# Kernel tuning notes

Measured on AMD Instinct MI355X. Metric: run time of the kernel, lower is better.

Reference implementation:

```python
import jax, jax.numpy as jnp
import numpy as np

B, Hg, Wg, DIM, HEADS, WS, SHIFT = 16, 64, 64, 512, 16, 8, 4
HIDDEN = 4 * DIM
PRIOR_BETA = 1.0
EPS = 1e-5


def _layernorm(x, g, b):
    m = jnp.mean(x, axis=-1, keepdims=True)
    v = jnp.mean(jnp.square(x - m), axis=-1, keepdims=True)
    return (x - m) / jnp.sqrt(v + EPS) * g + b


def _rel_pos_index(ws):
    coords = np.stack(np.meshgrid(np.arange(ws), np.arange(ws), indexing='ij')).reshape(2, -1)
    rel = (coords[:, :, None] - coords[:, None, :]).transpose(1, 2, 0)
    rel[..., 0] += ws - 1
    rel[..., 1] += ws - 1
    rel[..., 0] *= 2 * ws - 1
    return rel.sum(-1)  # (N, N) int


def _shift_mask(H, W, ws, shift):
    img = np.zeros((H, W))
    cnt = 0
    for hs in (slice(0, -ws), slice(-ws, -shift), slice(-shift, None)):
        for wsl in (slice(0, -ws), slice(-ws, -shift), slice(-shift, None)):
            img[hs, wsl] = cnt
            cnt += 1
    N = ws * ws
    mw = img.reshape(H // ws, ws, W // ws, ws).transpose(0, 2, 1, 3).reshape(-1, N)
    am = mw[:, None, :] - mw[:, :, None]
    return np.where(am != 0, -100.0, 0.0).astype(np.float32)  # (nW, N, N)


def setup_inputs() -> dict:
    key = jax.random.key(0)
    ks = jax.random.split(key, 8)
    s = 0.02
    return {
        'x': jax.random.normal(ks[0], (B, Hg * Wg, DIM), jnp.float32),
        'M_map': jax.random.uniform(ks[1], (B, Hg, Wg, 1), jnp.float32),
        'norm1_g': jnp.ones((DIM,), jnp.float32),
        'norm1_b': jnp.zeros((DIM,), jnp.float32),
        'qkv_w': jax.random.normal(ks[2], (3 * DIM, DIM), jnp.float32) * s,
        'qkv_b': jnp.zeros((3 * DIM,), jnp.float32),
        'proj_w': jax.random.normal(ks[3], (DIM, DIM), jnp.float32) * s,
        'proj_b': jnp.zeros((DIM,), jnp.float32),
        'rpb_table': jax.random.normal(ks[4], ((2 * WS - 1) ** 2, HEADS), jnp.float32) * s,
        'norm2_g': jnp.ones((DIM,), jnp.float32),
        'norm2_b': jnp.zeros((DIM,), jnp.float32),
        'fc1_w': jax.random.normal(ks[5], (HIDDEN, DIM), jnp.float32) * s,
        'fc1_b': jnp.zeros((HIDDEN,), jnp.float32),
        'fc2_w': jax.random.normal(ks[6], (DIM, HIDDEN), jnp.float32) * s,
        'fc2_b': jnp.zeros((DIM,), jnp.float32),
        'H': Hg,
        'W': Wg,
    }


def reference(x, M_map, norm1_g, norm1_b, qkv_w, qkv_b, proj_w, proj_b, rpb_table,
              norm2_g, norm2_b, fc1_w, fc1_b, fc2_w, fc2_b, H, W):
    Bsz, L, C = x.shape
    ws, shift, heads = WS, SHIFT, HEADS
    N = ws * ws
    hd = C // heads
    scale = hd ** -0.5

    shortcut = x
    y = _layernorm(x, norm1_g, norm1_b).reshape(Bsz, H, W, C)
    Mm = jnp.clip(M_map[..., 0], 0.0, 1.0)  # (B, H, W)

    # cyclic shift (SW-MSA)
    y = jnp.roll(y, (-shift, -shift), axis=(1, 2))
    Mm = jnp.roll(Mm, (-shift, -shift), axis=(1, 2))

    # window partition -> (B*nW, N, C) and (B*nW, N)
    def win_part(t):
        c = t.shape[-1]
        t = t.reshape(Bsz, H // ws, ws, W // ws, ws, c)
        return t.transpose(0, 1, 3, 2, 4, 5).reshape(-1, N, c)

    xw = win_part(y)
    mw = win_part(Mm[..., None])[..., 0]
    B_ = xw.shape[0]

    qkv = (xw @ qkv_w.T + qkv_b).reshape(B_, N, 3, heads, hd).transpose(2, 0, 3, 1, 4)
    q, k, v = qkv[0], qkv[1], qkv[2]  # each (B_, heads, N, hd)
    attn = jnp.einsum('bhnd,bhmd->bhnm', q * scale, k)

    # relative position bias (heads, N, N)
    rpi = _rel_pos_index(ws)
    rpb = rpb_table[rpi.reshape(-1)].reshape(N, N, heads).transpose(2, 0, 1)
    attn = attn + rpb[None]

    # semantic prior bias: 0.5*(M_i + M_j), broadcast over heads
    sb = 0.5 * (mw[:, :, None] + mw[:, None, :])  # (B_, N, N)
    attn = attn + PRIOR_BETA * sb[:, None]

    # shift mask
    am = jnp.asarray(_shift_mask(H, W, ws, shift), attn.dtype)  # (nW, N, N)
    nW = am.shape[0]
    attn = attn.reshape(Bsz, nW, heads, N, N) + am[None, :, None]
    attn = attn.reshape(B_, heads, N, N)

    attn = jax.nn.softmax(attn, axis=-1)
    out = jnp.einsum('bhnm,bhmd->bhnd', attn, v).transpose(0, 2, 1, 3).reshape(B_, N, C)
    out = out @ proj_w.T + proj_b

    # window reverse + reverse shift
    out = out.reshape(Bsz, H // ws, W // ws, ws, ws, C).transpose(0, 1, 3, 2, 4, 5).reshape(Bsz, H, W, C)
    out = jnp.roll(out, (shift, shift), axis=(1, 2)).reshape(Bsz, L, C)

    x1 = shortcut + out
    h = jax.nn.gelu(_layernorm(x1, norm2_g, norm2_b) @ fc1_w.T + fc1_b, approximate=False)
    return x1 + (h @ fc2_w.T + fc2_b)
```

## Files before the change

kernel.cpp:

```cpp
#include <hip/hip_runtime.h>
#include <hip/hip_bf16.h>

typedef unsigned short u16;
typedef unsigned int u32;
typedef __attribute__((ext_vector_type(4))) float f32x4;
typedef __attribute__((ext_vector_type(8))) short bf16x8;

#define DEV static __device__ __forceinline__

DEV float bf2f(u16 u) { u32 x = ((u32)u) << 16; return __builtin_bit_cast(float, x); }
DEV u16 f2bf(float f) {
  __hip_bfloat16 h = __float2bfloat16(f);
  return __builtin_bit_cast(u16, h);
}

DEV void gld16(const u16* g, u16* l) {
  __builtin_amdgcn_global_load_lds((const __attribute__((address_space(1))) void*)g,
                                   (__attribute__((address_space(3))) void*)l, 16, 0, 0);
}

__global__ void cvt_bf16(const float* __restrict__ s, u16* __restrict__ d, int n) {
  int i = blockIdx.x * 256 + threadIdx.x;
  if (i < n) d[i] = f2bf(s[i]);
}

__global__ __launch_bounds__(256)
void ln_bf16(const float* __restrict__ src, const float* __restrict__ g,
             const float* __restrict__ b, u16* __restrict__ dst) {
  const int row = blockIdx.x * 4 + (threadIdx.x >> 6);
  const int lane = threadIdx.x & 63;
  const float* p = src + (long)row * 512 + lane * 8;
  float x[8];
  *(float4*)&x[0] = *(const float4*)p;
  *(float4*)&x[4] = *(const float4*)(p + 4);
  float s = 0.f;
#pragma unroll
  for (int e = 0; e < 8; ++e) s += x[e];
#pragma unroll
  for (int off = 32; off; off >>= 1) s += __shfl_xor(s, off, 64);
  const float mean = s * (1.0f / 512.0f);
  float q = 0.f;
#pragma unroll
  for (int e = 0; e < 8; ++e) { float d = x[e] - mean; q += d * d; }
#pragma unroll
  for (int off = 32; off; off >>= 1) q += __shfl_xor(q, off, 64);
  const float rinv = rsqrtf(q * (1.0f / 512.0f) + 1e-5f);
  u16 o[8];
  const int c0 = lane * 8;
#pragma unroll
  for (int e = 0; e < 8; ++e) o[e] = f2bf((x[e] - mean) * rinv * g[c0 + e] + b[c0 + e]);
  *(uint4*)(dst + (long)row * 512 + c0) = *(uint4*)o;
}

enum { EPI_QKV = 0, EPI_PROJ = 1, EPI_GELU = 2, EPI_FC2 = 3 };

constexpr int SLOT = 12288;

template <int EPI>
__global__ __launch_bounds__(512, 4)
void gemm256(const u16* __restrict__ A, const u16* __restrict__ W,
             const float* __restrict__ bias, const float* __restrict__ res,
             void* __restrict__ outv, int M, int N, int K) {
  extern __shared__ u16 sm[];
  (void)M;
  const int t = threadIdx.x;
  const int lane = t & 63;
  const int wave = t >> 6;
  const int wm = wave >> 2;
  const int wn = wave & 3;
  const long m0 = (long)blockIdx.y * 128;
  const long n0 = (long)blockIdx.x * 256;

  const int sr = t >> 2;
  const int sc = ((t & 3) ^ ((sr >> 1) & 3)) * 8;
  const u16* gA0 = A + (m0 + sr) * (long)K + sc;
  const u16* gB0 = W + (n0 + sr) * (long)K + sc;
  const u16* gB1 = gB0 + 128L * K;
  u16* lws = sm + wave * 512;

  const int NT = K >> 5;
  f32x4 acc[4][4] = {};
  const int fr = lane & 15;
  const int kp = ((lane >> 4) ^ ((fr >> 1) & 3)) * 8;

#define STAGE(slot, tile)                      \
  do {                                         \
    const int _k = (tile) * 32;                \
    u16* _b = lws + (slot) * SLOT;             \
    gld16(gA0 + _k, _b);                       \
    gld16(gB0 + _k, _b + 4096);                \
    gld16(gB1 + _k, _b + 8192);                \
  } while (0)

#define COMPUTE(slot)                                                                           \
  do {                                                                                          \
    const u16* Ab = sm + (slot) * SLOT + (wm * 64 + fr) * 32 + kp;                              \
    const u16* Bb = sm + (slot) * SLOT + 4096 + (wn * 64 + fr) * 32 + kp;                       \
    bf16x8 af[4], bfv[4];                                                                       \
    _Pragma("unroll")                                                                           \
    for (int i = 0; i < 4; ++i) af[i] = *(const bf16x8*)(Ab + i * 512);                         \
    _Pragma("unroll")                                                                           \
    for (int j = 0; j < 4; ++j) bfv[j] = *(const bf16x8*)(Bb + j * 512);                        \
    __builtin_amdgcn_s_setprio(1);                                                              \
    _Pragma("unroll")                                                                           \
    for (int i = 0; i < 4; ++i)                                                                 \
      _Pragma("unroll")                                                                         \
      for (int j = 0; j < 4; ++j)                                                               \
        acc[i][j] = __builtin_amdgcn_mfma_f32_16x16x32_bf16(af[i], bfv[j], acc[i][j], 0, 0, 0); \
    __builtin_amdgcn_s_setprio(0);                                                              \
  } while (0)

  STAGE(0, 0);
  __syncthreads();

  int kt = 0;
  for (; kt < NT - 1; ++kt) {
    STAGE((kt + 1) & 1, kt + 1);
    COMPUTE(kt & 1);
    __syncthreads();
  }
  COMPUTE(kt & 1);
#undef STAGE
#undef COMPUTE

  const int col = lane & 15;
  const int rq = (lane >> 4) * 4;
#pragma unroll
  for (int mi = 0; mi < 4; ++mi) {
#pragma unroll
    for (int ni = 0; ni < 4; ++ni) {
#pragma unroll
      for (int r = 0; r < 4; ++r) {
        const long m = m0 + wm * 64 + mi * 16 + rq + r;
        const long n = n0 + wn * 64 + ni * 16 + col;
        const float v = acc[mi][ni][r] + bias[n];
        const long idx = m * (long)N + n;
        if constexpr (EPI == EPI_QKV) {
          ((u16*)outv)[idx] = f2bf(v);
        } else if constexpr (EPI == EPI_PROJ) {
          ((float*)outv)[idx] = v + res[idx];
        } else if constexpr (EPI == EPI_GELU) {
          ((u16*)outv)[idx] = f2bf(0.5f * v * (1.0f + erff(v * 0.70710678118f)));
        } else {
          ((float*)outv)[idx] = v + res[idx];
        }
      }
    }
  }
}

constexpr int SS_S = 68;
constexpr int VT_S = 72;

__global__ __launch_bounds__(256)
void attn_mfma(const u16* __restrict__ qkv, const float* __restrict__ mmap,
               const float* __restrict__ rpb, u16* __restrict__ outp) {
  __shared__ u16 SSb[4 * 64 * SS_S];
  __shared__ u16 Vtb[4 * 32 * VT_S];
  __shared__ u16 rpb_s[16 * 226];
  __shared__ float mw[64];
  __shared__ int tok[64];
  __shared__ int regi[64];

  const int t = threadIdx.x;
  const int lane = t & 63, wave = t >> 6;
  const int c = lane & 15, q = lane >> 4;
  const int win = blockIdx.x;
  const int b = win >> 6, wh = (win >> 3) & 7, ww = win & 7;

  if (t < 64) {
    const int i = t >> 3, j = t & 7;
    const int hs = wh * 8 + i, wsv = ww * 8 + j;
    const int h = (hs + 4) & 63, w = (wsv + 4) & 63;
    const int tk = b * 4096 + h * 64 + w;
    tok[t] = tk;
    mw[t] = fminf(fmaxf(mmap[tk], 0.f), 1.f);
    regi[t] = (hs < 56 ? 0 : (hs < 60 ? 1 : 2)) * 3 + (wsv < 56 ? 0 : (wsv < 60 ? 1 : 2));
  }
  for (int id = t; id < 3600; id += 256) {
    const int h = id & 15, idx = id >> 4;
    rpb_s[h * 226 + idx] = f2bf(rpb[id]);
  }
  __syncthreads();

  u16* SS = SSb + wave * 64 * SS_S;
  u16* Vt = Vtb + wave * 32 * VT_S;

  int tQ[4];
  float mwn[16], mwm[4];
  int rgn[16], rgm[4];
#pragma unroll
  for (int i = 0; i < 4; ++i) tQ[i] = tok[16 * i + c];
#pragma unroll
  for (int i = 0; i < 4; ++i)
#pragma unroll
    for (int r = 0; r < 4; ++r) {
      const int n = 16 * i + 4 * q + r;
      mwn[i * 4 + r] = mw[n];
      rgn[i * 4 + r] = regi[n];
    }
#pragma unroll
  for (int j = 0; j < 4; ++j) {
    const int m = 16 * j + c;
    mwm[j] = mw[m];
    rgm[j] = regi[m];
  }
  const int imc = c >> 3, jmc = c & 7;
  const int tV = tok[lane];
  const float scale = 0.17677669529663687f;

  for (int hi = 0; hi < 4; ++hi) {
    const int head = wave * 4 + hi;

    bf16x8 qf[4], kf[4];
#pragma unroll
    for (int i = 0; i < 4; ++i) {
      const u16* base = qkv + (long)tQ[i] * 1536 + head * 32 + q * 8;
      qf[i] = *(const bf16x8*)(base);
      kf[i] = *(const bf16x8*)(base + 512);
    }

    {
      const u16* vp = qkv + (long)tV * 1536 + 1024 + head * 32;
      u16 vv[32];
      *(uint4*)&vv[0]  = *(const uint4*)(vp);
      *(uint4*)&vv[8]  = *(const uint4*)(vp + 8);
      *(uint4*)&vv[16] = *(const uint4*)(vp + 16);
      *(uint4*)&vv[24] = *(const uint4*)(vp + 24);
#pragma unroll
      for (int d = 0; d < 32; ++d) Vt[d * VT_S + lane] = vv[d];
    }

    f32x4 acc[4][4] = {};
#pragma unroll
    for (int i = 0; i < 4; ++i)
#pragma unroll
      for (int j = 0; j < 4; ++j)
        acc[i][j] = __builtin_amdgcn_mfma_f32_16x16x32_bf16(qf[i], kf[j], acc[i][j], 0, 0, 0);

    const u16* rb = rpb_s + head * 226;
    float rmx[16], rsum[16];
#pragma unroll
    for (int i = 0; i < 4; ++i)
#pragma unroll
      for (int r = 0; r < 4; ++r) {
        const int n = 16 * i + 4 * q + r;
        const int inr = n >> 3, jnr = n & 7;
        float mx = -1e30f;
#pragma unroll
        for (int j = 0; j < 4; ++j) {
          const int di = inr - 2 * j - imc + 7;
          const int dj = jnr - jmc + 7;
          float s = acc[i][j][r] * scale + bf2f(rb[di * 15 + dj]) +
                    0.5f * (mwn[i * 4 + r] + mwm[j]);
          if (rgn[i * 4 + r] != rgm[j]) s -= 100.f;
          acc[i][j][r] = s;
          mx = fmaxf(mx, s);
        }
        rmx[i * 4 + r] = mx;
      }
#pragma unroll
    for (int ir = 0; ir < 16; ++ir)
#pragma unroll
      for (int msk = 1; msk < 16; msk <<= 1)
        rmx[ir] = fmaxf(rmx[ir], __shfl_xor(rmx[ir], msk, 64));
#pragma unroll
    for (int i = 0; i < 4; ++i)
#pragma unroll
      for (int r = 0; r < 4; ++r) {
        float sm = 0.f;
#pragma unroll
        for (int j = 0; j < 4; ++j) {
          const float e = __expf(acc[i][j][r] - rmx[i * 4 + r]);
          acc[i][j][r] = e;
          sm += e;
        }
        rsum[i * 4 + r] = sm;
      }
#pragma unroll
    for (int ir = 0; ir < 16; ++ir) {
#pragma unroll
      for (int msk = 1; msk < 16; msk <<= 1)
        rsum[ir] += __shfl_xor(rsum[ir], msk, 64);
      rsum[ir] = 1.0f / rsum[ir];
    }

#pragma unroll
    for (int i = 0; i < 4; ++i)
#pragma unroll
      for (int j = 0; j < 4; ++j) {
        ushort4 pk;
        pk.x = f2bf(acc[i][j][0] * rsum[i * 4 + 0]);
        pk.y = f2bf(acc[i][j][1] * rsum[i * 4 + 1]);
        pk.z = f2bf(acc[i][j][2] * rsum[i * 4 + 2]);
        pk.w = f2bf(acc[i][j][3] * rsum[i * 4 + 3]);
        *(ushort4*)&SS[(16 * j + c) * SS_S + 16 * i + 4 * q] = pk;
      }

    __syncthreads();

    bf16x8 av[2][2];
#pragma unroll
    for (int mi = 0; mi < 2; ++mi)
#pragma unroll
      for (int ki = 0; ki < 2; ++ki)
        av[mi][ki] = *(const bf16x8*)&Vt[(16 * mi + c) * VT_S + 32 * ki + 8 * q];

    f32x4 oacc[2][4] = {};
#pragma unroll
    for (int ki = 0; ki < 2; ++ki)
#pragma unroll
      for (int ni = 0; ni < 4; ++ni) {
        union { u16 h[8]; bf16x8 v; } ub;
#pragma unroll
        for (int jj = 0; jj < 8; ++jj)
          ub.h[jj] = SS[(32 * ki + 8 * q + jj) * SS_S + 16 * ni + c];
#pragma unroll
        for (int mi = 0; mi < 2; ++mi)
          oacc[mi][ni] = __builtin_amdgcn_mfma_f32_16x16x32_bf16(av[mi][ki], ub.v, oacc[mi][ni], 0, 0, 0);
      }

#pragma unroll
    for (int ni = 0; ni < 4; ++ni) {
      u16* ob = outp + (long)tQ[ni] * 512 + head * 32;
#pragma unroll
      for (int mi = 0; mi < 2; ++mi) {
        ushort4 pk;
        pk.x = f2bf(oacc[mi][ni][0]);
        pk.y = f2bf(oacc[mi][ni][1]);
        pk.z = f2bf(oacc[mi][ni][2]);
        pk.w = f2bf(oacc[mi][ni][3]);
        *(ushort4*)(ob + 16 * mi + 4 * q) = pk;
      }
    }
    __syncthreads();
  }
}

extern "C" void kernel_launch(void* const* d_in, const int* in_sizes, int n_in,
                              void* d_out, int out_size, void* d_ws, size_t ws_size,
                              hipStream_t stream) {
  (void)in_sizes; (void)n_in; (void)out_size; (void)ws_size;
  const float* x      = (const float*)d_in[0];
  const float* mmap   = (const float*)d_in[1];
  const float* n1g    = (const float*)d_in[2];
  const float* n1b    = (const float*)d_in[3];
  const float* qkv_w  = (const float*)d_in[4];
  const float* qkv_b  = (const float*)d_in[5];
  const float* proj_w = (const float*)d_in[6];
  const float* proj_b = (const float*)d_in[7];
  const float* rpb    = (const float*)d_in[8];
  const float* n2g    = (const float*)d_in[9];
  const float* n2b    = (const float*)d_in[10];
  const float* fc1_w  = (const float*)d_in[11];
  const float* fc1_b  = (const float*)d_in[12];
  const float* fc2_w  = (const float*)d_in[13];
  const float* fc2_b  = (const float*)d_in[14];
  float* out = (float*)d_out;
  char* ws = (char*)d_ws;

  u16*   ybf   = (u16*)(ws);
  u16*   qkvbf = (u16*)(ws + (64L  << 20));
  u16*   attno = (u16*)(ws + (256L << 20));
  float* x1    = (float*)(ws + (320L << 20));
  u16*   hbuf  = qkvbf;
  u16*   wqkv  = (u16*)(ws + (448L << 20));
  u16*   wproj = wqkv + 1536 * 512;
  u16*   wfc1  = wproj + 512 * 512;
  u16*   wfc2  = wfc1 + 2048 * 512;

  static bool smem_init = false;
  if (!smem_init) {
    smem_init = true;
    (void)hipFuncSetAttribute(reinterpret_cast<const void*>(gemm256<EPI_QKV>),
                              hipFuncAttributeMaxDynamicSharedMemorySize, 49152);
    (void)hipFuncSetAttribute(reinterpret_cast<const void*>(gemm256<EPI_PROJ>),
                              hipFuncAttributeMaxDynamicSharedMemorySize, 49152);
    (void)hipFuncSetAttribute(reinterpret_cast<const void*>(gemm256<EPI_GELU>),
                              hipFuncAttributeMaxDynamicSharedMemorySize, 49152);
    (void)hipFuncSetAttribute(reinterpret_cast<const void*>(gemm256<EPI_FC2>),
                              hipFuncAttributeMaxDynamicSharedMemorySize, 49152);
  }

  cvt_bf16<<<1536 * 512 / 256, 256, 0, stream>>>(qkv_w, wqkv, 1536 * 512);
  cvt_bf16<<<512 * 512 / 256, 256, 0, stream>>>(proj_w, wproj, 512 * 512);
  cvt_bf16<<<2048 * 512 / 256, 256, 0, stream>>>(fc1_w, wfc1, 2048 * 512);
  cvt_bf16<<<512 * 2048 / 256, 256, 0, stream>>>(fc2_w, wfc2, 512 * 2048);

  ln_bf16<<<16384, 256, 0, stream>>>(x, n1g, n1b, ybf);
  gemm256<EPI_QKV><<<dim3(6, 512), 512, 49152, stream>>>(ybf, wqkv, qkv_b, nullptr, qkvbf, 65536, 1536, 512);
  attn_mfma<<<1024, 256, 0, stream>>>(qkvbf, mmap, rpb, attno);
  gemm256<EPI_PROJ><<<dim3(2, 512), 512, 49152, stream>>>(attno, wproj, proj_b, x, x1, 65536, 512, 512);
  ln_bf16<<<16384, 256, 0, stream>>>(x1, n2g, n2b, ybf);
  gemm256<EPI_GELU><<<dim3(8, 512), 512, 49152, stream>>>(ybf, wfc1, fc1_b, nullptr, hbuf, 65536, 2048, 512);
  gemm256<EPI_FC2><<<dim3(2, 512), 512, 49152, stream>>>(hbuf, wfc2, fc2_b, x1, out, 65536, 512, 2048);
}
```

Before: 1.050 ms.

## Triple-buffer GEMM K-loop with vmcnt waits and use fast GELU approximation

Converts the GEMM main loop from double to triple buffering in LDS, prefetching two K-tiles ahead. A partial s_waitcnt vmcnt plus a raw barrier replaces the full __syncthreads, so global loads overlap compute. The epilogue hoists bias loads and replaces erff with an Abramowitz-Stegun polynomial GELU using a fast reciprocal and exp, which cuts transcendental cost but slightly lowers accuracy. Dynamic shared memory rises to 72KB per block, which may reduce occupancy.

```diff
diff --git a/kernel.cpp b/kernel.cpp
--- a/kernel.cpp
+++ b/kernel.cpp
@@ -12,6 +12,18 @@
 DEV u16 f2bf(float f) {
   __hip_bfloat16 h = __float2bfloat16(f);
   return __builtin_bit_cast(u16, h);
+}
+
+DEV float fast_gelu(float x) {
+  const float ax = fabsf(x) * 0.70710678118f;
+  const float t = __builtin_amdgcn_rcpf(1.0f + 0.3275911f * ax);
+  const float poly =
+      t * (0.254829592f +
+           t * (-0.284496736f + t * (1.421413741f + t * (-1.453152027f + t * 1.061405429f))));
+  const float e = __expf(-ax * ax);
+  float er = 1.0f - poly * e;
+  er = __builtin_copysignf(er, x);
+  return 0.5f * x * (1.0f + er);
 }
 
 DEV void gld16(const u16* g, u16* l) {
@@ -111,39 +123,61 @@
   } while (0)
 
   STAGE(0, 0);
-  __syncthreads();
-
+  STAGE(1, 1);
+  asm volatile("s_waitcnt vmcnt(3)" ::: "memory");
+  __builtin_amdgcn_s_barrier();
+  asm volatile("" ::: "memory");
+
+  int cs = 0, ss = 2;
   int kt = 0;
-  for (; kt < NT - 1; ++kt) {
-    STAGE((kt + 1) & 1, kt + 1);
-    COMPUTE(kt & 1);
-    __syncthreads();
-  }
-  COMPUTE(kt & 1);
+  for (; kt < NT - 2; ++kt) {
+    STAGE(ss, kt + 2);
+    COMPUTE(cs);
+    asm volatile("s_waitcnt vmcnt(3)" ::: "memory");
+    __builtin_amdgcn_s_barrier();
+    asm volatile("" ::: "memory");
+    cs = cs == 2 ? 0 : cs + 1;
+    ss = ss == 2 ? 0 : ss + 1;
+  }
+  COMPUTE(cs);
+  asm volatile("s_waitcnt vmcnt(0)" ::: "memory");
+  __builtin_amdgcn_s_barrier();
+  asm volatile("" ::: "memory");
+  cs = cs == 2 ? 0 : cs + 1;
+  COMPUTE(cs);
 #undef STAGE
 #undef COMPUTE
 
   const int col = lane & 15;
   const int rq = (lane >> 4) * 4;
+  const long ncol = n0 + wn * 64 + col;
+  float bv[4];
+#pragma unroll
+  for (int ni = 0; ni < 4; ++ni) bv[ni] = bias[ncol + ni * 16];
 #pragma unroll
   for (int mi = 0; mi < 4; ++mi) {
 #pragma unroll
-    for (int ni = 0; ni < 4; ++ni) {
-#pragma unroll
-      for (int r = 0; r < 4; ++r) {
-        const long m = m0 + wm * 64 + mi * 16 + rq + r;
-        const long n = n0 + wn * 64 + ni * 16 + col;
-        const float v = acc[mi][ni][r] + bias[n];
-        const long idx = m * (long)N + n;
-        if constexpr (EPI == EPI_QKV) {
-          ((u16*)outv)[idx] = f2bf(v);
-        } else if constexpr (EPI == EPI_PROJ) {
-          ((float*)outv)[idx] = v + res[idx];
-        } else if constexpr (EPI == EPI_GELU) {
-          ((u16*)outv)[idx] = f2bf(0.5f * v * (1.0f + erff(v * 0.70710678118f)));
-        } else {
-          ((float*)outv)[idx] = v + res[idx];
-        }
+    for (int r = 0; r < 4; ++r) {
+      const long m = m0 + wm * 64 + mi * 16 + rq + r;
+      const long base = m * (long)N + ncol;
+      if constexpr (EPI == EPI_QKV) {
+        u16* p = (u16*)outv + base;
+#pragma unroll
+        for (int ni = 0; ni < 4; ++ni) p[ni * 16] = f2bf(acc[mi][ni][r] + bv[ni]);
+      } else if constexpr (EPI == EPI_PROJ) {
+        float* p = (float*)outv + base;
+        const float* rp = res + base;
+#pragma unroll
+        for (int ni = 0; ni < 4; ++ni) p[ni * 16] = acc[mi][ni][r] + bv[ni] + rp[ni * 16];
+      } else if constexpr (EPI == EPI_GELU) {
+        u16* p = (u16*)outv + base;
+#pragma unroll
+        for (int ni = 0; ni < 4; ++ni) p[ni * 16] = f2bf(fast_gelu(acc[mi][ni][r] + bv[ni]));
+      } else {
+        float* p = (float*)outv + base;
+        const float* rp = res + base;
+#pragma unroll
+        for (int ni = 0; ni < 4; ++ni) p[ni * 16] = acc[mi][ni][r] + bv[ni] + rp[ni * 16];
       }
     }
   }
@@ -373,13 +407,13 @@
   if (!smem_init) {
     smem_init = true;
     (void)hipFuncSetAttribute(reinterpret_cast<const void*>(gemm256<EPI_QKV>),
-                              hipFuncAttributeMaxDynamicSharedMemorySize, 49152);
+                              hipFuncAttributeMaxDynamicSharedMemorySize, 73728);
     (void)hipFuncSetAttribute(reinterpret_cast<const void*>(gemm256<EPI_PROJ>),
-                              hipFuncAttributeMaxDynamicSharedMemorySize, 49152);
+                              hipFuncAttributeMaxDynamicSharedMemorySize, 73728);
     (void)hipFuncSetAttribute(reinterpret_cast<const void*>(gemm256<EPI_GELU>),
-                              hipFuncAttributeMaxDynamicSharedMemorySize, 49152);
+                              hipFuncAttributeMaxDynamicSharedMemorySize, 73728);
     (void)hipFuncSetAttribute(reinterpret_cast<const void*>(gemm256<EPI_FC2>),
-                              hipFuncAttributeMaxDynamicSharedMemorySize, 49152);
+                              hipFuncAttributeMaxDynamicSharedMemorySize, 73728);
   }
 
   cvt_bf16<<<1536 * 512 / 256, 256, 0, stream>>>(qkv_w, wqkv, 1536 * 512);
@@ -388,10 +422,10 @@
   cvt_bf16<<<512 * 2048 / 256, 256, 0, stream>>>(fc2_w, wfc2, 512 * 2048);
 
   ln_bf16<<<16384, 256, 0, stream>>>(x, n1g, n1b, ybf);
-  gemm256<EPI_QKV><<<dim3(6, 512), 512, 49152, stream>>>(ybf, wqkv, qkv_b, nullptr, qkvbf, 65536, 1536, 512);
+  gemm256<EPI_QKV><<<dim3(6, 512), 512, 73728, stream>>>(ybf, wqkv, qkv_b, nullptr, qkvbf, 65536, 1536, 512);
   attn_mfma<<<1024, 256, 0, stream>>>(qkvbf, mmap, rpb, attno);
-  gemm256<EPI_PROJ><<<dim3(2, 512), 512, 49152, stream>>>(attno, wproj, proj_b, x, x1, 65536, 512, 512);
+  gemm256<EPI_PROJ><<<dim3(2, 512), 512, 73728, stream>>>(attno, wproj, proj_b, x, x1, 65536, 512, 512);
   ln_bf16<<<16384, 256, 0, stream>>>(x1, n2g, n2b, ybf);
-  gemm256<EPI_GELU><<<dim3(8, 512), 512, 49152, stream>>>(ybf, wfc1, fc1_b, nullptr, hbuf, 65536, 2048, 512);
-  gemm256<EPI_FC2><<<dim3(2, 512), 512, 49152, stream>>>(hbuf, wfc2, fc2_b, x1, out, 65536, 512, 2048);
-}
+  gemm256<EPI_GELU><<<dim3(8, 512), 512, 73728, stream>>>(ybf, wfc1, fc1_b, nullptr, hbuf, 65536, 2048, 512);
+  gemm256<EPI_FC2><<<dim3(2, 512), 512, 73728, stream>>>(hbuf, wfc2, fc2_b, x1, out, 65536, 512, 2048);
+}
```

After: 1.047 ms. Within noise of the previous version (-0.3%).
